# Performance work log

Hardware: AMD Instinct MI355X
Metric: run time of the kernel (lower is better)

The kernel has to match this reference:

```python
import jax, jax.numpy as jnp
import numpy as np

EPS = 1e-6
NUM_HEADS = 16

def _ln(x):
    m = jnp.mean(x, -1, keepdims=True)
    v = jnp.mean((x - m) ** 2, -1, keepdims=True)
    return (x - m) * jax.lax.rsqrt(v + EPS)

def _rms(x, w):
    return x * jax.lax.rsqrt(jnp.mean(x * x, -1, keepdims=True) + EPS) * w

def _to_mha(t):
    B, S, D = t.shape
    return t.reshape(B, S, NUM_HEADS, D // NUM_HEADS).transpose(0, 2, 1, 3)

def _rope(t, freqs):
    # t: [B,H,T,Hd], freqs: [T, Hd//2, 2] (cos, sin)
    B, H, T, Hd = t.shape
    tr = t.reshape(B, H, T, Hd // 2, 2)
    cos, sin = freqs[..., 0], freqs[..., 1]
    r = tr[..., 0] * cos - tr[..., 1] * sin
    i = tr[..., 0] * sin + tr[..., 1] * cos
    return jnp.stack([r, i], -1).reshape(B, H, T, Hd)

def _pre(h, qk_w, qn, kn, v_w, v_b):
    qk = h @ qk_w.T                      # [B,S,2D], no bias (c_qk bias=False)
    q, k = jnp.split(qk, 2, -1)
    q = _rms(_to_mha(q), qn)             # per-head RMSNorm
    k = _rms(_to_mha(k), kn)
    v = _to_mha(h @ v_w.T + v_b)
    return q, k, v

def _post(x, a, pw, pb, w1, b1, w3, b3, w2, b2):
    x = x + a @ pw.T + pb                # residual + c_proj
    h = _ln(x)
    m = (jax.nn.silu(h @ w1.T + b1) * (h @ w3.T + b3)) @ w2.T + b2  # SwiGLU
    return x + m

def _forward(x, c, freqs, px_qk_w, px_qn, px_kn, px_v_w, px_v_b,
             pc_qk_w, pc_qn, pc_kn, pc_v_w, pc_v_b,
             p1_proj_w, p1_proj_b, p1_w1, p1_b1, p1_w3, p1_b3, p1_w2, p1_b2,
             p2_proj_w, p2_proj_b, p2_w1, p2_b1, p2_w3, p2_b3, p2_w2, p2_b2):
    x_ln, c_ln = _ln(x), _ln(c)
    qc, kc, vc = _pre(c_ln, pc_qk_w, pc_qn, pc_kn, pc_v_w, pc_v_b)
    qx, kx, vx = _pre(x_ln, px_qk_w, px_qn, px_kn, px_v_w, px_v_b)
    q = jnp.concatenate([qc, qx], 2)     # [B,H,T,Hd], T = S+L
    k = jnp.concatenate([kc, kx], 2)
    v = jnp.concatenate([vc, vx], 2)
    q = _rope(q, freqs)
    k = _rope(k, freqs)
    Hd = q.shape[-1]
    scores = jnp.einsum('bhqd,bhkd->bhqk', q, k) / jnp.sqrt(jnp.float32(Hd))
    T = scores.shape[-1]
    causal = jnp.tril(jnp.ones((T, T), bool))
    scores = jnp.where(causal, scores, jnp.finfo(scores.dtype).min)
    p = jax.nn.softmax(scores, -1)
    y = jnp.einsum('bhqk,bhkd->bhqd', p, v)
    B, D = x.shape[0], x.shape[-1]
    y = y.transpose(0, 2, 1, 3).reshape(B, -1, D)  # [B,T,D]
    S = c.shape[1]
    y_c, y_x = y[:, :S], y[:, S:]
    x_out = _post(x, y_x, p1_proj_w, p1_proj_b, p1_w1, p1_b1, p1_w3, p1_b3, p1_w2, p1_b2)
    c_out = _post(c, y_c, p2_proj_w, p2_proj_b, p2_w1, p2_b1, p2_w3, p2_b3, p2_w2, p2_b2)
    return x_out, c_out

def setup_inputs() -> dict:
    B, L, S, D, H, FF = 1, 1536, 512, 1024, 16, 4096
    Hd, T = D // H, L + S
    key = jax.random.key(0)
    ks = iter(jax.random.split(key, 40))
    def rn(shape, s=0.02):
        return (jax.random.normal(next(ks), shape, jnp.float32) * s)
    pos = jnp.arange(T, dtype=jnp.float32)
    inv = 1.0 / (10000.0 ** (jnp.arange(0, Hd, 2, dtype=jnp.float32) / Hd))
    ang = pos[:, None] * inv[None, :]
    freqs = jnp.stack([jnp.cos(ang), jnp.sin(ang)], -1)  # [T, Hd//2, 2]
    inp = {
        'x': jax.random.normal(next(ks), (B, L, D), jnp.float32),
        'c': jax.random.normal(next(ks), (B, S, D), jnp.float32),
        'freqs': freqs,
        'px_qk_w': rn((2 * D, D)), 'px_qn': jnp.ones((Hd,)), 'px_kn': jnp.ones((Hd,)),
        'px_v_w': rn((D, D)), 'px_v_b': rn((D,)),
        'pc_qk_w': rn((2 * D, D)), 'pc_qn': jnp.ones((Hd,)), 'pc_kn': jnp.ones((Hd,)),
        'pc_v_w': rn((D, D)), 'pc_v_b': rn((D,)),
    }
    for pfx in ('p1', 'p2'):
        inp[pfx + '_proj_w'] = rn((D, D)); inp[pfx + '_proj_b'] = rn((D,))
        inp[pfx + '_w1'] = rn((FF, D)); inp[pfx + '_b1'] = rn((FF,))
        inp[pfx + '_w3'] = rn((FF, D)); inp[pfx + '_b3'] = rn((FF,))
        inp[pfx + '_w2'] = rn((D, FF)); inp[pfx + '_b2'] = rn((D,))
    return inp

def reference(x, c, freqs, px_qk_w, px_qn, px_kn, px_v_w, px_v_b,
              pc_qk_w, pc_qn, pc_kn, pc_v_w, pc_v_b,
              p1_proj_w, p1_proj_b, p1_w1, p1_b1, p1_w3, p1_b3, p1_w2, p1_b2,
              p2_proj_w, p2_proj_b, p2_w1, p2_b1, p2_w3, p2_b3, p2_w2, p2_b2):
    return _forward(x, c, freqs, px_qk_w, px_qn, px_kn, px_v_w, px_v_b,
                    pc_qk_w, pc_qn, pc_kn, pc_v_w, pc_v_b,
                    p1_proj_w, p1_proj_b, p1_w1, p1_b1, p1_w3, p1_b3, p1_w2, p1_b2,
                    p2_proj_w, p2_proj_b, p2_w1, p2_b1, p2_w3, p2_b3, p2_w2, p2_b2)
```

## Files before the change

### kernel.cpp

```cpp
#include <hip/hip_runtime.h>

typedef __attribute__((ext_vector_type(8))) short short8;
typedef __attribute__((ext_vector_type(4))) float floatx4;
typedef __attribute__((ext_vector_type(4))) unsigned short ushortx4;

__device__ __forceinline__ float bf2f(unsigned short u) {
  union { unsigned int i; float f; } v; v.i = ((unsigned int)u) << 16; return v.f;
}
__device__ __forceinline__ unsigned short f2bf(float f) {
  union { float f; unsigned int i; } v; v.f = f;
  unsigned int x = v.i + 0x7fffu + ((v.i >> 16) & 1u);
  return (unsigned short)(x >> 16);
}
__device__ __forceinline__ float loadE(const void* p, size_t i, int f) {
  return f ? ((const float*)p)[i] : bf2f(((const unsigned short*)p)[i]);
}
__device__ __forceinline__ uint4 packbf(float4 a, float4 b) {
  union { unsigned short u[8]; uint4 v; } p;
  p.u[0] = f2bf(a.x); p.u[1] = f2bf(a.y); p.u[2] = f2bf(a.z); p.u[3] = f2bf(a.w);
  p.u[4] = f2bf(b.x); p.u[5] = f2bf(b.y); p.u[6] = f2bf(b.z); p.u[7] = f2bf(b.w);
  return p.v;
}

__device__ __forceinline__ void gl16(const unsigned short* g, unsigned short* l) {
  __builtin_amdgcn_global_load_lds(
      (const __attribute__((address_space(1))) void*)g,
      (__attribute__((address_space(3))) void*)l, 16, 0, 0);
}

__global__ void detect_kernel(const unsigned int* __restrict__ probe, int* __restrict__ flag) {
  if (threadIdx.x == 0 && blockIdx.x == 0) *flag = (probe[0] == 0x3F800000u) ? 1 : 0;
}

struct CArgs {
  const void* in[12];
  unsigned short* out[12];
  unsigned int cum[12];
};
__global__ __launch_bounds__(256) void convw_kernel(CArgs a, int total_chunks,
                                                    const int* __restrict__ flagp) {
  const int flag = *flagp;
  for (int c = blockIdx.x * 256 + threadIdx.x; c < total_chunks; c += gridDim.x * 256) {
    int s = 0;
    while (c >= (int)a.cum[s]) ++s;
    unsigned int base = s ? a.cum[s - 1] : 0u;
    size_t e = (size_t)(c - base) * 8;
    if (flag) {
      const float* in = (const float*)a.in[s] + e;
      float4 v0 = *(const float4*)in;
      float4 v1 = *(const float4*)(in + 4);
      *(uint4*)(a.out[s] + e) = packbf(v0, v1);
    } else {
      *(uint4*)(a.out[s] + e) = *(const uint4*)((const unsigned short*)a.in[s] + e);
    }
  }
}

__global__ __launch_bounds__(256) void zero_kernel(void* __restrict__ out, int out_elems,
                                                   const int* __restrict__ flagp) {
  int limit = (*flagp) ? (out_elems >> 2) : (out_elems >> 3);
  int i = blockIdx.x * 256 + threadIdx.x;
  if (i < limit) ((uint4*)out)[i] = make_uint4(0, 0, 0, 0);
}

__global__ __launch_bounds__(256) void reduce_kernel(const float* __restrict__ part,
                                                     const unsigned short* __restrict__ mid,
                                                     const void* __restrict__ b1,
                                                     const void* __restrict__ b2,
                                                     float* __restrict__ out,
                                                     const int* __restrict__ flagp) {
  if (!*flagp) return;
  const size_t TD = 2097152, LD = (size_t)1536 * 1024, SD = (size_t)512 * 1024;
  size_t i = ((size_t)blockIdx.x * 256 + threadIdx.x) * 4;
  if (i >= TD) return;
  float4 v  = *(const float4*)(part + i);
  float4 v1 = *(const float4*)(part + TD + i);
  float4 v2 = *(const float4*)(part + 2 * TD + i);
  float4 v3 = *(const float4*)(part + 3 * TD + i);
  v.x += v1.x + v2.x + v3.x;
  v.y += v1.y + v2.y + v3.y;
  v.z += v1.z + v2.z + v3.z;
  v.w += v1.w + v2.w + v3.w;
  int col = (int)(i & 1023);
  const float* bias = (const float*)((i < LD) ? b1 : b2);
  size_t ri = (i < LD) ? (SD + i) : (i - LD);
  v.x += bias[col + 0] + bf2f(mid[ri + 0]);
  v.y += bias[col + 1] + bf2f(mid[ri + 1]);
  v.z += bias[col + 2] + bf2f(mid[ri + 2]);
  v.w += bias[col + 3] + bf2f(mid[ri + 3]);
  *(float4*)(out + i) = v;
}

__global__ __launch_bounds__(256) void ln_ext_kernel(const void* __restrict__ cin,
                                                     const void* __restrict__ xin,
                                                     unsigned short* __restrict__ out,
                                                     const int* __restrict__ flagp) {
  const int D = 1024, S = 512;
  const int flag = *flagp;
  int row = blockIdx.x;
  const void* src = (row < S) ? cin : xin;
  size_t rb = (size_t)(row < S ? row : row - S) * D;
  int base = threadIdx.x * 4;
  float x0 = loadE(src, rb + base + 0, flag);
  float x1 = loadE(src, rb + base + 1, flag);
  float x2 = loadE(src, rb + base + 2, flag);
  float x3 = loadE(src, rb + base + 3, flag);
  float s1 = x0 + x1 + x2 + x3;
  float s2 = x0 * x0 + x1 * x1 + x2 * x2 + x3 * x3;
  for (int off = 32; off; off >>= 1) {
    s1 += __shfl_down(s1, off, 64);
    s2 += __shfl_down(s2, off, 64);
  }
  __shared__ float red[8];
  int wid = threadIdx.x >> 6;
  if ((threadIdx.x & 63) == 0) { red[wid] = s1; red[4 + wid] = s2; }
  __syncthreads();
  s1 = red[0] + red[1] + red[2] + red[3];
  s2 = red[4] + red[5] + red[6] + red[7];
  float mean = s1 * (1.0f / D);
  float var = s2 * (1.0f / D) - mean * mean;
  float inv = rsqrtf(var + 1e-6f);
  unsigned short* dst = out + (size_t)row * D + base;
  dst[0] = f2bf((x0 - mean) * inv);
  dst[1] = f2bf((x1 - mean) * inv);
  dst[2] = f2bf((x2 - mean) * inv);
  dst[3] = f2bf((x3 - mean) * inv);
}

__global__ __launch_bounds__(256) void ln_mid_kernel(const unsigned short* __restrict__ in,
                                                     unsigned short* __restrict__ outc,
                                                     unsigned short* __restrict__ outx) {
  const int D = 1024, S = 512;
  int row = blockIdx.x;
  const unsigned short* src = in + (size_t)row * D;
  int base = threadIdx.x * 4;
  float x0 = bf2f(src[base + 0]);
  float x1 = bf2f(src[base + 1]);
  float x2 = bf2f(src[base + 2]);
  float x3 = bf2f(src[base + 3]);
  float s1 = x0 + x1 + x2 + x3;
  float s2 = x0 * x0 + x1 * x1 + x2 * x2 + x3 * x3;
  for (int off = 32; off; off >>= 1) {
    s1 += __shfl_down(s1, off, 64);
    s2 += __shfl_down(s2, off, 64);
  }
  __shared__ float red[8];
  int wid = threadIdx.x >> 6;
  if ((threadIdx.x & 63) == 0) { red[wid] = s1; red[4 + wid] = s2; }
  __syncthreads();
  s1 = red[0] + red[1] + red[2] + red[3];
  s2 = red[4] + red[5] + red[6] + red[7];
  float mean = s1 * (1.0f / D);
  float var = s2 * (1.0f / D) - mean * mean;
  float inv = rsqrtf(var + 1e-6f);
  unsigned short* dst = (row < S ? outc + (size_t)row * D : outx + (size_t)(row - S) * D) + base;
  dst[0] = f2bf((x0 - mean) * inv);
  dst[1] = f2bf((x1 - mean) * inv);
  dst[2] = f2bf((x2 - mean) * inv);
  dst[3] = f2bf((x3 - mean) * inv);
}

struct GArgs {
  const unsigned short* A[4];
  const void* B[4];
  const void* bias[4];
  const void* res[4];
  void* C[4];
  unsigned long long oo[4];
  int mcum[4];
  int N[4];
  int K;
  int nd;
  int tmask;
  float* part;
};

#define BAR() asm volatile("s_waitcnt lgkmcnt(0)\n\ts_barrier" ::: "memory")
#define FBAR() asm volatile("s_waitcnt vmcnt(0) lgkmcnt(0)\n\ts_barrier" ::: "memory")
#define CBAR4() asm volatile("s_waitcnt vmcnt(4) lgkmcnt(0)\n\ts_barrier" ::: "memory")

template <int RES_MODE, int OUT_MODE, int SPLITK, int BBF16>
__global__ __launch_bounds__(256) void gemm_kernel(GArgs g, const int* __restrict__ flagp) {
  const int flag = *flagp;
  int by = blockIdx.y;
  int d = 0;
  while (d < g.nd - 1 && by >= g.mcum[d]) ++d;
  int mbase = (d == 0) ? 0 : g.mcum[d - 1];
  const int m0 = (by - mbase) * 128;
  const int N = g.N[d];
  const int n0 = blockIdx.x * 128;
  if (n0 >= N) return;
  const int K = g.K;
  int kbeg = 0, kend = K;
  if (SPLITK > 1) {
    if (!flag) {
      if (blockIdx.z != 0) return;
    } else {
      int kl = K / SPLITK;
      kbeg = blockIdx.z * kl;
      kend = kbeg + kl;
    }
  }
  const int nt = (kend - kbeg) >> 5;

  constexpr int NBUF = BBF16 ? 3 : 2;
  constexpr int BSTRIDE = BBF16 ? 4096 : 5120;
  __shared__ __align__(16) unsigned short sA[NBUF * BSTRIDE];
  __shared__ __align__(16) unsigned short sB[NBUF * BSTRIDE];

  const int tid = threadIdx.x;
  const int lane = tid & 63;
  const int wave = tid >> 6;
  const int wm = (wave >> 1) * 64, wn = (wave & 1) * 64;
  const int srow = tid >> 2;
  const int scol = BBF16 ? ((((tid & 3) ^ ((tid >> 3) & 3))) * 8) : ((tid & 3) * 8);
  const unsigned short* Ag0 = g.A[d] + (size_t)(m0 + srow) * K + kbeg + scol;
  const unsigned short* Ag1 = Ag0 + (size_t)64 * K;
  const unsigned short* Bh0 = (const unsigned short*)g.B[d] + (size_t)(n0 + srow) * K + kbeg + scol;
  const unsigned short* Bh1 = Bh0 + (size_t)64 * K;

  const int fr = lane & 15;
  const int rdo = BBF16 ? ((((lane >> 4) ^ ((fr >> 1) & 3))) * 8) : ((lane >> 4) * 8);
  constexpr int PITCH = BBF16 ? 32 : 40;
  floatx4 acc[4][4] = {};
  auto compute = [&](const unsigned short* as, const unsigned short* bs) {
    short8 af[4], bfr[4];
    #pragma unroll
    for (int i = 0; i < 4; ++i) {
      af[i]  = *(const short8*)(as + (wm + i * 16 + fr) * PITCH + rdo);
      bfr[i] = *(const short8*)(bs + (wn + i * 16 + fr) * PITCH + rdo);
    }
    #pragma unroll
    for (int mi = 0; mi < 4; ++mi)
      #pragma unroll
      for (int ni = 0; ni < 4; ++ni)
        acc[mi][ni] = __builtin_amdgcn_mfma_f32_16x16x32_bf16(af[mi], bfr[ni], acc[mi][ni], 0, 0, 0);
  };

  if (BBF16) {
    unsigned short* lA0 = sA + wave * 512;
    unsigned short* lA1 = lA0 + 2048;
    unsigned short* lB0 = sB + wave * 512;
    unsigned short* lB1 = lB0 + 2048;
    auto stage = [&](int buf, int kk) {
      int bo = buf * 4096;
      gl16(Ag0 + kk, lA0 + bo);
      gl16(Ag1 + kk, lA1 + bo);
      gl16(Bh0 + kk, lB0 + bo);
      gl16(Bh1 + kk, lB1 + bo);
    };
    stage(0, 0);
    if (nt > 1) stage(1, 32);
    int b = 0;
    for (int t = 0; t < nt; ++t) {
      if (t + 1 < nt) CBAR4();
      else            FBAR();
      int b2 = (b >= 1) ? b - 1 : 2;
      if (t + 2 < nt) stage(b2, (t + 2) * 32);
      compute(sA + b * 4096, sB + b * 4096);
      b = (b == 2) ? 0 : b + 1;
    }
  } else {
    const float* Bf0 = (const float*)g.B[d] + (size_t)(n0 + srow) * K + kbeg + scol;
    const float* Bf1 = Bf0 + (size_t)64 * K;
    const int wo0 = srow * 40 + scol;
    const int wo1 = wo0 + 64 * 40;
    uint4 ra0, ra1, rb0, rb1;
    auto load_tile = [&](int kk) {
      ra0 = *(const uint4*)(Ag0 + kk);
      ra1 = *(const uint4*)(Ag1 + kk);
      if (!flag) {
        rb0 = *(const uint4*)(Bh0 + kk);
        rb1 = *(const uint4*)(Bh1 + kk);
      } else {
        float4 x0 = *(const float4*)(Bf0 + kk), x1 = *(const float4*)(Bf0 + kk + 4);
        float4 y0 = *(const float4*)(Bf1 + kk), y1 = *(const float4*)(Bf1 + kk + 4);
        rb0 = packbf(x0, x1);
        rb1 = packbf(y0, y1);
      }
    };
    auto store_tile = [&](int buf) {
      unsigned short* sa = sA + buf * 5120;
      unsigned short* sb = sB + buf * 5120;
      *(uint4*)(sa + wo0) = ra0;
      *(uint4*)(sa + wo1) = ra1;
      *(uint4*)(sb + wo0) = rb0;
      *(uint4*)(sb + wo1) = rb1;
    };
    load_tile(0);
    store_tile(0);
    if (nt > 1) load_tile(32);
    BAR();
    for (int t = 0; t < nt; ++t) {
      if (t + 1 < nt) {
        store_tile((t + 1) & 1);
        if (t + 2 < nt) load_tile((t + 2) * 32);
      }
      compute(sA + (t & 1) * 5120, sB + (t & 1) * 5120);
      if (t + 1 < nt) BAR();
    }
  }

  const void* bias = g.bias[d];
  const void* res = g.res[d];
  void* C = g.C[d];
  const size_t oo = g.oo[d];
  const bool first = (SPLITK <= 1) || (blockIdx.z == 0) || !flag;
  const bool rawpart = (OUT_MODE == 3) && (flag != 0);
  const bool trans = (OUT_MODE == 0) && (((g.tmask) >> d) & 1);
  #pragma unroll
  for (int mi = 0; mi < 4; ++mi)
    #pragma unroll
    for (int ni = 0; ni < 4; ++ni) {
      int colb = n0 + wn + ni * 16 + (lane & 15);
      int rowb = m0 + wm + mi * 16 + (lane >> 4) * 4;
      if (trans) {
        ushortx4 o4;
        #pragma unroll
        for (int r = 0; r < 4; ++r) {
          float val = acc[mi][ni][r];
          if (bias) val += loadE(bias, (size_t)colb, flag);
          o4[r] = f2bf(val);
        }
        *(ushortx4*)((unsigned short*)C + (size_t)colb * 2048 + oo + rowb) = o4;
      } else {
        #pragma unroll
        for (int r = 0; r < 4; ++r) {
          int row = rowb + r;
          int col = colb;
          float val = acc[mi][ni][r];
          size_t off = (size_t)row * N + col;
          if (first && !rawpart) {
            if (bias) val += loadE(bias, (size_t)col, flag);
            if (RES_MODE == 1) val += loadE(res, off, flag);
            if (RES_MODE == 3) {
              float h1v = bf2f(((const unsigned short*)res)[off]);
              val = (h1v / (1.0f + __expf(-h1v))) * val;
            }
            if (RES_MODE == 4) val += bf2f(((const unsigned short*)res)[off]);
          }
          if (OUT_MODE == 0) {
            ((unsigned short*)C)[off] = f2bf(val);
          } else if (OUT_MODE == 3) {
            if (flag) g.part[(size_t)blockIdx.z * 2097152 + oo + off] = val;
            else      ((unsigned short*)C)[oo + off] = f2bf(val);
          } else {
            if (flag) {
              if (SPLITK > 1) atomicAdd((float*)C + oo + off, val);
              else            ((float*)C)[oo + off] = val;
            } else {
              ((unsigned short*)C)[oo + off] = f2bf(val);
            }
          }
        }
      }
    }
}

__global__ __launch_bounds__(256) void rmsrope_kernel(
    unsigned short* __restrict__ qk,
    const void* __restrict__ qn_c, const void* __restrict__ kn_c,
    const void* __restrict__ qn_x, const void* __restrict__ kn_x,
    const void* __restrict__ freqs, const int* __restrict__ flagp) {
  const int flag = *flagp;
  int t = blockIdx.x;
  int h = blockIdx.y * 4 + (threadIdx.x >> 6);
  int d = threadIdx.x & 63;
  unsigned short* qrow = qk + (size_t)t * 2048 + h * 64;
  unsigned short* krow = qrow + 1024;
  float q = bf2f(qrow[d]), k = bf2f(krow[d]);
  float qs = q * q, ks = k * k;
  for (int off = 32; off; off >>= 1) {
    qs += __shfl_xor(qs, off, 64);
    ks += __shfl_xor(ks, off, 64);
  }
  const void* qn = (t < 512) ? qn_c : qn_x;
  const void* kn = (t < 512) ? kn_c : kn_x;
  q = q * rsqrtf(qs * (1.0f / 64.0f) + 1e-6f) * loadE(qn, d, flag);
  k = k * rsqrtf(ks * (1.0f / 64.0f) + 1e-6f) * loadE(kn, d, flag);
  int j = d >> 1;
  float cv = loadE(freqs, (size_t)(t * 32 + j) * 2 + 0, flag);
  float sv = loadE(freqs, (size_t)(t * 32 + j) * 2 + 1, flag);
  float qo = __shfl_xor(q, 1, 64);
  float ko = __shfl_xor(k, 1, 64);
  float qn2, kn2;
  if ((d & 1) == 0) { qn2 = q * cv - qo * sv; kn2 = k * cv - ko * sv; }
  else              { qn2 = qo * sv + q * cv; kn2 = ko * sv + k * cv; }
  qrow[d] = f2bf(qn2);
  krow[d] = f2bf(kn2);
}

__global__ __launch_bounds__(256) void attn_kernel(const unsigned short* __restrict__ qk,
                                                   const unsigned short* __restrict__ vT,
                                                   unsigned short* __restrict__ y) {
  int id = blockIdx.x;
  int blk = (id & 256) ? (31 - (id & 31)) : (id & 31);
  int h = (id >> 5) & 15;
  int wv = threadIdx.x >> 6;
  int lane = threadIdx.x & 63;
  int qbase = blk * 64 + wv * 16;

  __shared__ __align__(16) unsigned short Ks[2 * 4096];
  __shared__ __align__(16) unsigned short Vs[2 * 4096];
  __shared__ __align__(16) unsigned short ps[4][16 * 72];

  const int c0 = wv * 64 + lane;
  const int r0 = c0 >> 3,         k0 = (c0 & 7) ^ (r0 & 7);
  const int r1 = (c0 + 256) >> 3, k1 = (c0 & 7) ^ (r1 & 7);
  unsigned short* kd0 = Ks + wv * 512;
  unsigned short* kd1 = Ks + 2048 + wv * 512;
  unsigned short* vd0 = Vs + wv * 512;
  unsigned short* vd1 = Vs + 2048 + wv * 512;
  const unsigned short* kgp0 = qk + 1024 + h * 64 + k0 * 8 + (size_t)r0 * 2048;
  const unsigned short* kgp1 = qk + 1024 + h * 64 + k1 * 8 + (size_t)r1 * 2048;
  const unsigned short* vgp0 = vT + (size_t)(h * 64 + r0) * 2048 + k0 * 8;
  const unsigned short* vgp1 = vT + (size_t)(h * 64 + r1) * 2048 + k1 * 8;
  auto stage = [&](int buf, int j0) {
    int bo = buf * 4096;
    gl16(kgp0 + (size_t)j0 * 2048, kd0 + bo);
    gl16(kgp1 + (size_t)j0 * 2048, kd1 + bo);
    gl16(vgp0 + j0, vd0 + bo);
    gl16(vgp1 + j0, vd1 + bo);
  };

  short8 qa[2];
  {
    int m = lane & 15, dj = (lane >> 4) * 8;
    const unsigned short* qp = qk + (size_t)(qbase + m) * 2048 + h * 64 + dj;
    qa[0] = *(const short8*)(qp);
    qa[1] = *(const short8*)(qp + 32);
  }
  floatx4 o[4] = {};
  float mrow[4] = {-1e30f, -1e30f, -1e30f, -1e30f};
  float lrow[4] = {0.f, 0.f, 0.f, 0.f};
  int ntiles = blk + 1;

  stage(0, 0);
  FBAR();
  for (int tile = 0; tile < ntiles; ++tile) {
    int j0 = tile * 64;
    if (tile + 1 < ntiles) stage((tile + 1) & 1, j0 + 64);
    const unsigned short* Kb = Ks + (tile & 1) * 4096;
    const unsigned short* Vb = Vs + (tile & 1) * 4096;
    floatx4 sacc[4];
    #pragma unroll
    for (int kg = 0; kg < 4; ++kg) {
      floatx4 z = {0.f, 0.f, 0.f, 0.f};
      #pragma unroll
      for (int kc = 0; kc < 2; ++kc) {
        int kr = kg * 16 + (lane & 15);
        int p = (kc * 4 + (lane >> 4)) ^ (kr & 7);
        short8 kb = *(const short8*)(Kb + kr * 64 + p * 8);
        z = __builtin_amdgcn_mfma_f32_16x16x32_bf16(qa[kc], kb, z, 0, 0, 0);
      }
      sacc[kg] = z;
    }
    if (tile == blk) {
      #pragma unroll
      for (int kg = 0; kg < 4; ++kg)
        #pragma unroll
        for (int r = 0; r < 4; ++r) {
          int key_g = j0 + kg * 16 + (lane & 15);
          int q_g = qbase + (lane >> 4) * 4 + r;
          float s = sacc[kg][r] * 0.125f;
          sacc[kg][r] = (key_g <= q_g) ? s : -1e30f;
        }
    } else {
      #pragma unroll
      for (int kg = 0; kg < 4; ++kg)
        #pragma unroll
        for (int r = 0; r < 4; ++r) sacc[kg][r] *= 0.125f;
    }
    #pragma unroll
    for (int r = 0; r < 4; ++r) {
      float mx = fmaxf(fmaxf(sacc[0][r], sacc[1][r]), fmaxf(sacc[2][r], sacc[3][r]));
      mx = fmaxf(mx, __shfl_xor(mx, 1, 64));
      mx = fmaxf(mx, __shfl_xor(mx, 2, 64));
      mx = fmaxf(mx, __shfl_xor(mx, 4, 64));
      mx = fmaxf(mx, __shfl_xor(mx, 8, 64));
      float mnew = fmaxf(mrow[r], mx);
      float al = __expf(mrow[r] - mnew);
      mrow[r] = mnew;
      float sum = 0.f;
      #pragma unroll
      for (int kg = 0; kg < 4; ++kg) {
        float p = __expf(sacc[kg][r] - mnew);
        sacc[kg][r] = p;
        sum += p;
      }
      sum += __shfl_xor(sum, 1, 64);
      sum += __shfl_xor(sum, 2, 64);
      sum += __shfl_xor(sum, 4, 64);
      sum += __shfl_xor(sum, 8, 64);
      lrow[r] = lrow[r] * al + sum;
      #pragma unroll
      for (int ni = 0; ni < 4; ++ni) o[ni][r] *= al;
    }
    unsigned short* pw = ps[wv];
    #pragma unroll
    for (int kg = 0; kg < 4; ++kg)
      #pragma unroll
      for (int r = 0; r < 4; ++r)
        pw[((lane >> 4) * 4 + r) * 72 + kg * 16 + (lane & 15)] = f2bf(sacc[kg][r]);
    asm volatile("s_waitcnt lgkmcnt(0)" ::: "memory");
    short8 pa[2];
    pa[0] = *(const short8*)(pw + (lane & 15) * 72 + (lane >> 4) * 8);
    pa[1] = *(const short8*)(pw + (lane & 15) * 72 + 32 + (lane >> 4) * 8);
    #pragma unroll
    for (int ni = 0; ni < 4; ++ni) {
      floatx4 z = o[ni];
      int dd = ni * 16 + (lane & 15);
      #pragma unroll
      for (int kc = 0; kc < 2; ++kc) {
        int p = (kc * 4 + (lane >> 4)) ^ (dd & 7);
        short8 vb = *(const short8*)(Vb + dd * 64 + p * 8);
        z = __builtin_amdgcn_mfma_f32_16x16x32_bf16(pa[kc], vb, z, 0, 0, 0);
      }
      o[ni] = z;
    }
    if (tile + 1 < ntiles) FBAR();
  }
  #pragma unroll
  for (int ni = 0; ni < 4; ++ni)
    #pragma unroll
    for (int r = 0; r < 4; ++r) {
      int q = qbase + (lane >> 4) * 4 + r;
      int dd = ni * 16 + (lane & 15);
      y[(size_t)q * 1024 + h * 64 + dd] = f2bf(o[ni][r] / lrow[r]);
    }
}

extern "C" void kernel_launch(void* const* d_in, const int* in_sizes, int n_in,
                              void* d_out, int out_size, void* d_ws, size_t ws_size,
                              hipStream_t stream) {
  const int L = 1536, S = 512, D = 1024, T = 2048, FF = 4096;
  const void* x        = d_in[0];
  const void* c        = d_in[1];
  const void* freqs    = d_in[2];
  const void* px_qk_w  = d_in[3];
  const void* px_qn    = d_in[4];
  const void* px_kn    = d_in[5];
  const void* px_v_w   = d_in[6];
  const void* px_v_b   = d_in[7];
  const void* pc_qk_w  = d_in[8];
  const void* pc_qn    = d_in[9];
  const void* pc_kn    = d_in[10];
  const void* pc_v_w   = d_in[11];
  const void* pc_v_b   = d_in[12];
  const void* p1_proj_w = d_in[13];
  const void* p1_proj_b = d_in[14];
  const void* p1_w1 = d_in[15];
  const void* p1_b1 = d_in[16];
  const void* p1_w3 = d_in[17];
  const void* p1_b3 = d_in[18];
  const void* p1_w2 = d_in[19];
  const void* p1_b2 = d_in[20];
  const void* p2_proj_w = d_in[21];
  const void* p2_proj_b = d_in[22];
  const void* p2_w1 = d_in[23];
  const void* p2_b1 = d_in[24];
  const void* p2_w3 = d_in[25];
  const void* p2_b3 = d_in[26];
  const void* p2_w2 = d_in[27];
  const void* p2_b2 = d_in[28];

  char* ws = (char*)d_ws;
  unsigned short* hln     = (unsigned short*)(ws);
  unsigned short* ybuf    = (unsigned short*)(ws);
  unsigned short* h1c     = (unsigned short*)(ws);
  unsigned short* qkbuf   = (unsigned short*)(ws + ((size_t)4  << 20));
  unsigned short* h1x     = (unsigned short*)(ws + ((size_t)4  << 20));
  unsigned short* vbufT   = (unsigned short*)(ws + ((size_t)12 << 20));
  unsigned short* mid     = (unsigned short*)(ws + ((size_t)16 << 20));
  unsigned short* midln_c = (unsigned short*)(ws + ((size_t)20 << 20));
  int*            flag    = (int*)(ws + ((size_t)21 << 20));
  unsigned short* midln_x = (unsigned short*)d_out;
  unsigned short* hlnx    = hln + (size_t)S * D;

  const bool conv = ws_size >= ((size_t)90 << 20);
  unsigned short* wbf = (unsigned short*)(ws + ((size_t)24 << 20));
  unsigned short* b_qk_c = wbf + 0;
  unsigned short* b_qk_x = wbf + 2097152;
  unsigned short* b_v_c  = wbf + 4194304;
  unsigned short* b_v_x  = wbf + 5242880;
  unsigned short* b_pj1  = wbf + 6291456;
  unsigned short* b_pj2  = wbf + 7340032;
  unsigned short* b_w1p1 = wbf + 8388608;
  unsigned short* b_w1p2 = wbf + 12582912;
  unsigned short* b_w3p1 = wbf + 16777216;
  unsigned short* b_w3p2 = wbf + 20971520;
  unsigned short* b_w2p1 = wbf + 25165824;
  unsigned short* b_w2p2 = wbf + 29360128;
  float* part = (float*)(ws + ((size_t)40 << 20));

  detect_kernel<<<1, 64, 0, stream>>>((const unsigned int*)px_qn, flag);

  if (conv) {
    CArgs ca;
    const void* ins[12]   = {pc_qk_w, px_qk_w, pc_v_w, px_v_w, p1_proj_w, p2_proj_w,
                             p1_w1, p2_w1, p1_w3, p2_w3, p1_w2, p2_w2};
    unsigned short* os[12] = {b_qk_c, b_qk_x, b_v_c, b_v_x, b_pj1, b_pj2,
                              b_w1p1, b_w1p2, b_w3p1, b_w3p2, b_w2p1, b_w2p2};
    unsigned int cnt[12]  = {262144, 262144, 131072, 131072, 131072, 131072,
                             524288, 524288, 524288, 524288, 524288, 524288};
    unsigned int cum = 0;
    for (int i = 0; i < 12; ++i) { ca.in[i] = ins[i]; ca.out[i] = os[i]; cum += cnt[i]; ca.cum[i] = cum; }
    convw_kernel<<<2048, 256, 0, stream>>>(ca, (int)cum, flag);
  }

  ln_ext_kernel<<<T, 256, 0, stream>>>(c, x, hln, flag);

  {
    GArgs g = {};
    g.A[0] = hln;  g.bias[0] = nullptr; g.C[0] = qkbuf;                    g.mcum[0] = 4;  g.N[0] = 2048;
    g.A[1] = hlnx; g.bias[1] = nullptr; g.C[1] = qkbuf + (size_t)S * 2048; g.mcum[1] = 16; g.N[1] = 2048;
    g.A[2] = hln;  g.bias[2] = pc_v_b;  g.C[2] = vbufT; g.oo[2] = 0;       g.mcum[2] = 20; g.N[2] = 1024;
    g.A[3] = hlnx; g.bias[3] = px_v_b;  g.C[3] = vbufT; g.oo[3] = S;       g.mcum[3] = 32; g.N[3] = 1024;
    g.K = 1024; g.nd = 4; g.tmask = 0b1100;
    if (conv) {
      g.B[0] = b_qk_c; g.B[1] = b_qk_x; g.B[2] = b_v_c; g.B[3] = b_v_x;
      gemm_kernel<0, 0, 1, 1><<<dim3(16, 32), 256, 0, stream>>>(g, flag);
    } else {
      g.B[0] = pc_qk_w; g.B[1] = px_qk_w; g.B[2] = pc_v_w; g.B[3] = px_v_w;
      gemm_kernel<0, 0, 1, 0><<<dim3(16, 32), 256, 0, stream>>>(g, flag);
    }
  }
  rmsrope_kernel<<<dim3(T, 4), 256, 0, stream>>>(qkbuf, pc_qn, pc_kn, px_qn, px_kn, freqs, flag);
  attn_kernel<<<512, 256, 0, stream>>>(qkbuf, vbufT, ybuf);

  {
    GArgs g = {};
    g.A[0] = ybuf;                  g.bias[0] = p2_proj_b; g.res[0] = c; g.C[0] = mid;                  g.mcum[0] = 4;  g.N[0] = 1024;
    g.A[1] = ybuf + (size_t)S * D;  g.bias[1] = p1_proj_b; g.res[1] = x; g.C[1] = mid + (size_t)S * D;  g.mcum[1] = 16; g.N[1] = 1024;
    g.K = 1024; g.nd = 2;
    if (conv) {
      g.B[0] = b_pj2; g.B[1] = b_pj1;
      gemm_kernel<1, 0, 1, 1><<<dim3(8, 16), 256, 0, stream>>>(g, flag);
    } else {
      g.B[0] = p2_proj_w; g.B[1] = p1_proj_w;
      gemm_kernel<1, 0, 1, 0><<<dim3(8, 16), 256, 0, stream>>>(g, flag);
    }
  }
  ln_mid_kernel<<<T, 256, 0, stream>>>(mid, midln_c, midln_x);

  {
    GArgs g = {};
    g.A[0] = midln_x; g.bias[0] = p1_b1; g.C[0] = h1x; g.mcum[0] = 12; g.N[0] = 4096;
    g.A[1] = midln_c; g.bias[1] = p2_b1; g.C[1] = h1c; g.mcum[1] = 16; g.N[1] = 4096;
    g.K = 1024; g.nd = 2;
    if (conv) {
      g.B[0] = b_w1p1; g.B[1] = b_w1p2;
      gemm_kernel<0, 0, 1, 1><<<dim3(32, 16), 256, 0, stream>>>(g, flag);
    } else {
      g.B[0] = p1_w1; g.B[1] = p2_w1;
      gemm_kernel<0, 0, 1, 0><<<dim3(32, 16), 256, 0, stream>>>(g, flag);
    }
  }
  {
    GArgs g = {};
    g.A[0] = midln_x; g.bias[0] = p1_b3; g.res[0] = h1x; g.C[0] = h1x; g.mcum[0] = 12; g.N[0] = 4096;
    g.A[1] = midln_c; g.bias[1] = p2_b3; g.res[1] = h1c; g.C[1] = h1c; g.mcum[1] = 16; g.N[1] = 4096;
    g.K = 1024; g.nd = 2;
    if (conv) {
      g.B[0] = b_w3p1; g.B[1] = b_w3p2;
      gemm_kernel<3, 0, 1, 1><<<dim3(32, 16), 256, 0, stream>>>(g, flag);
    } else {
      g.B[0] = p1_w3; g.B[1] = p2_w3;
      gemm_kernel<3, 0, 1, 0><<<dim3(32, 16), 256, 0, stream>>>(g, flag);
    }
  }
  if (conv) {
    GArgs g = {};
    g.A[0] = h1x; g.bias[0] = p1_b2; g.res[0] = mid + (size_t)S * D; g.C[0] = d_out; g.oo[0] = 0;             g.mcum[0] = 12; g.N[0] = 1024;
    g.A[1] = h1c; g.bias[1] = p2_b2; g.res[1] = mid;                 g.C[1] = d_out; g.oo[1] = (size_t)L * D; g.mcum[1] = 16; g.N[1] = 1024;
    g.K = 4096; g.nd = 2;
    g.part = part;
    g.B[0] = b_w2p1; g.B[1] = b_w2p2;
    gemm_kernel<4, 3, 4, 1><<<dim3(8, 16, 4), 256, 0, stream>>>(g, flag);
    reduce_kernel<<<2048, 256, 0, stream>>>(part, mid, p1_b2, p2_b2, (float*)d_out, flag);
  } else {
    zero_kernel<<<2048, 256, 0, stream>>>(d_out, out_size, flag);
    GArgs g = {};
    g.A[0] = h1x; g.bias[0] = p1_b2; g.res[0] = mid + (size_t)S * D; g.C[0] = d_out; g.oo[0] = 0;             g.mcum[0] = 12; g.N[0] = 1024;
    g.A[1] = h1c; g.bias[1] = p2_b2; g.res[1] = mid;                 g.C[1] = d_out; g.oo[1] = (size_t)L * D; g.mcum[1] = 16; g.N[1] = 1024;
    g.K = 4096; g.nd = 2;
    g.B[0] = p1_w2; g.B[1] = p2_w2;
    gemm_kernel<4, 2, 4, 0><<<dim3(8, 16, 4), 256, 0, stream>>>(g, flag);
  }
}
```

Baseline: 495.6 us.

## Split-K the projection GEMM, split weight conversion, and unroll the conversion kernel

```diff
diff --git a/kernel.cpp b/kernel.cpp
--- a/kernel.cpp
+++ b/kernel.cpp
@@ -37,21 +37,33 @@
   unsigned short* out[12];
   unsigned int cum[12];
 };
-__global__ __launch_bounds__(256) void convw_kernel(CArgs a, int total_chunks,
-                                                    const int* __restrict__ flagp) {
+__global__ __launch_bounds__(256) void convw_kernel(CArgs a, const int* __restrict__ flagp) {
   const int flag = *flagp;
-  for (int c = blockIdx.x * 256 + threadIdx.x; c < total_chunks; c += gridDim.x * 256) {
-    int s = 0;
-    while (c >= (int)a.cum[s]) ++s;
-    unsigned int base = s ? a.cum[s - 1] : 0u;
-    size_t e = (size_t)(c - base) * 8;
-    if (flag) {
-      const float* in = (const float*)a.in[s] + e;
-      float4 v0 = *(const float4*)in;
-      float4 v1 = *(const float4*)(in + 4);
-      *(uint4*)(a.out[s] + e) = packbf(v0, v1);
-    } else {
-      *(uint4*)(a.out[s] + e) = *(const uint4*)((const unsigned short*)a.in[s] + e);
+  int bc = blockIdx.x * 2048;
+  int s = 0;
+  while (bc >= (int)a.cum[s]) ++s;
+  int base = s ? (int)a.cum[s - 1] : 0;
+  size_t e0 = ((size_t)(bc - base) + threadIdx.x) * 8;
+  if (flag) {
+    const float* in = (const float*)a.in[s];
+    unsigned short* out = a.out[s];
+    float4 v0[8], v1[8];
+    #pragma unroll
+    for (int k = 0; k < 8; ++k) {
+      size_t e = e0 + (size_t)k * 2048;
+      v0[k] = *(const float4*)(in + e);
+      v1[k] = *(const float4*)(in + e + 4);
+    }
+    #pragma unroll
+    for (int k = 0; k < 8; ++k)
+      *(uint4*)(out + e0 + (size_t)k * 2048) = packbf(v0[k], v1[k]);
+  } else {
+    const unsigned short* in = (const unsigned short*)a.in[s];
+    unsigned short* out = a.out[s];
+    #pragma unroll
+    for (int k = 0; k < 8; ++k) {
+      size_t e = e0 + (size_t)k * 2048;
+      *(uint4*)(out + e) = *(const uint4*)(in + e);
     }
   }
 }
@@ -89,6 +101,40 @@
   v.z += bias[col + 2] + bf2f(mid[ri + 2]);
   v.w += bias[col + 3] + bf2f(mid[ri + 3]);
   *(float4*)(out + i) = v;
+}
+
+__global__ __launch_bounds__(256) void reduce_mid_kernel(const float* __restrict__ part,
+                                                         const void* __restrict__ cres,
+                                                         const void* __restrict__ xres,
+                                                         const float* __restrict__ b_c,
+                                                         const float* __restrict__ b_x,
+                                                         unsigned short* __restrict__ mid,
+                                                         const int* __restrict__ flagp) {
+  if (!*flagp) return;
+  const size_t TD = 2097152;
+  size_t i = ((size_t)blockIdx.x * 256 + threadIdx.x) * 4;
+  if (i >= TD) return;
+  float4 v  = *(const float4*)(part + i);
+  float4 v1 = *(const float4*)(part + TD + i);
+  float4 v2 = *(const float4*)(part + 2 * TD + i);
+  float4 v3 = *(const float4*)(part + 3 * TD + i);
+  v.x += v1.x + v2.x + v3.x;
+  v.y += v1.y + v2.y + v3.y;
+  v.z += v1.z + v2.z + v3.z;
+  v.w += v1.w + v2.w + v3.w;
+  int row = (int)(i >> 10), col = (int)(i & 1023);
+  const float* bias = (row < 512) ? b_c : b_x;
+  const float* res = (row < 512)
+      ? (const float*)cres + ((size_t)row << 10) + col
+      : (const float*)xres + ((size_t)(row - 512) << 10) + col;
+  float4 rv = *(const float4*)res;
+  float4 bv = *(const float4*)(bias + col);
+  ushortx4 o;
+  o[0] = f2bf(v.x + bv.x + rv.x);
+  o[1] = f2bf(v.y + bv.y + rv.y);
+  o[2] = f2bf(v.z + bv.z + rv.z);
+  o[3] = f2bf(v.w + bv.w + rv.w);
+  *(ushortx4*)(mid + i) = o;
 }
 
 __global__ __launch_bounds__(256) void ln_ext_kernel(const void* __restrict__ cin,
@@ -596,16 +642,17 @@
   detect_kernel<<<1, 64, 0, stream>>>((const unsigned int*)px_qn, flag);
 
   if (conv) {
-    CArgs ca;
-    const void* ins[12]   = {pc_qk_w, px_qk_w, pc_v_w, px_v_w, p1_proj_w, p2_proj_w,
-                             p1_w1, p2_w1, p1_w3, p2_w3, p1_w2, p2_w2};
-    unsigned short* os[12] = {b_qk_c, b_qk_x, b_v_c, b_v_x, b_pj1, b_pj2,
-                              b_w1p1, b_w1p2, b_w3p1, b_w3p2, b_w2p1, b_w2p2};
-    unsigned int cnt[12]  = {262144, 262144, 131072, 131072, 131072, 131072,
-                             524288, 524288, 524288, 524288, 524288, 524288};
+    CArgs ca = {};
+    const void* insA[8]    = {pc_qk_w, px_qk_w, pc_v_w, px_v_w, p1_proj_w, p2_proj_w,
+                              p1_w2, p2_w2};
+    unsigned short* osA[8] = {b_qk_c, b_qk_x, b_v_c, b_v_x, b_pj1, b_pj2,
+                              b_w2p1, b_w2p2};
+    unsigned int cntA[8]   = {262144, 262144, 131072, 131072, 131072, 131072,
+                              524288, 524288};
     unsigned int cum = 0;
-    for (int i = 0; i < 12; ++i) { ca.in[i] = ins[i]; ca.out[i] = os[i]; cum += cnt[i]; ca.cum[i] = cum; }
-    convw_kernel<<<2048, 256, 0, stream>>>(ca, (int)cum, flag);
+    for (int i = 0; i < 8; ++i) { ca.in[i] = insA[i]; ca.out[i] = osA[i]; cum += cntA[i]; ca.cum[i] = cum; }
+    for (int i = 8; i < 12; ++i) ca.cum[i] = 0x7FFFFFFFu;
+    convw_kernel<<<1024, 256, 0, stream>>>(ca, flag);
   }
 
   ln_ext_kernel<<<T, 256, 0, stream>>>(c, x, hln, flag);
@@ -628,18 +675,30 @@
   rmsrope_kernel<<<dim3(T, 4), 256, 0, stream>>>(qkbuf, pc_qn, pc_kn, px_qn, px_kn, freqs, flag);
   attn_kernel<<<512, 256, 0, stream>>>(qkbuf, vbufT, ybuf);
 
-  {
+  if (conv) {
+    GArgs g = {};
+    g.A[0] = ybuf;                  g.C[0] = mid; g.oo[0] = 0;             g.bias[0] = p2_proj_b; g.res[0] = c; g.mcum[0] = 4;  g.N[0] = 1024;
+    g.A[1] = ybuf + (size_t)S * D;  g.C[1] = mid; g.oo[1] = (size_t)S * D; g.bias[1] = p1_proj_b; g.res[1] = x; g.mcum[1] = 16; g.N[1] = 1024;
+    g.K = 1024; g.nd = 2;
+    g.part = part;
+    g.B[0] = b_pj2; g.B[1] = b_pj1;
+    gemm_kernel<1, 3, 4, 1><<<dim3(8, 16, 4), 256, 0, stream>>>(g, flag);
+    reduce_mid_kernel<<<2048, 256, 0, stream>>>(part, c, x, (const float*)p2_proj_b,
+                                                (const float*)p1_proj_b, mid, flag);
+    CArgs cb = {};
+    const void* insB[4]    = {p1_w1, p2_w1, p1_w3, p2_w3};
+    unsigned short* osB[4] = {b_w1p1, b_w1p2, b_w3p1, b_w3p2};
+    unsigned int cum = 0;
+    for (int i = 0; i < 4; ++i) { cb.in[i] = insB[i]; cb.out[i] = osB[i]; cum += 524288u; cb.cum[i] = cum; }
+    for (int i = 4; i < 12; ++i) cb.cum[i] = 0x7FFFFFFFu;
+    convw_kernel<<<1024, 256, 0, stream>>>(cb, flag);
+  } else {
     GArgs g = {};
     g.A[0] = ybuf;                  g.bias[0] = p2_proj_b; g.res[0] = c; g.C[0] = mid;                  g.mcum[0] = 4;  g.N[0] = 1024;
     g.A[1] = ybuf + (size_t)S * D;  g.bias[1] = p1_proj_b; g.res[1] = x; g.C[1] = mid + (size_t)S * D;  g.mcum[1] = 16; g.N[1] = 1024;
     g.K = 1024; g.nd = 2;
-    if (conv) {
-      g.B[0] = b_pj2; g.B[1] = b_pj1;
-      gemm_kernel<1, 0, 1, 1><<<dim3(8, 16), 256, 0, stream>>>(g, flag);
-    } else {
-      g.B[0] = p2_proj_w; g.B[1] = p1_proj_w;
-      gemm_kernel<1, 0, 1, 0><<<dim3(8, 16), 256, 0, stream>>>(g, flag);
-    }
+    g.B[0] = p2_proj_w; g.B[1] = p1_proj_w;
+    gemm_kernel<1, 0, 1, 0><<<dim3(8, 16), 256, 0, stream>>>(g, flag);
   }
   ln_mid_kernel<<<T, 256, 0, stream>>>(mid, midln_c, midln_x);
 
```

New measurement: 485.6 us. 1.02x faster.
